# Kernel optimization log

Hardware: AMD Instinct MI355X
Metric: run time of the kernel (lower is better)

The kernel has to match this reference:

```python
import jax, jax.numpy as jnp
import numpy as np
from jax import lax

# program token ids
PAD, START, END, SCENE, INTERSECT, FILT, RELATE, QUERY = range(8)
SKIP = (PAD, START, END)


def conv2d(x, w, b, dil=1):
    # 'same' padding for odd kernels (3x3 pad=dil, 1x1 pad=0), NCHW/OIHW
    pad = dil * (w.shape[2] // 2)
    y = lax.conv_general_dilated(x, w, (1, 1), [(pad, pad), (pad, pad)],
                                 rhs_dilation=(dil, dil),
                                 dimension_numbers=('NCHW', 'OIHW', 'NCHW'))
    return y + b[None, :, None, None]


def maxpool2(x):
    return lax.reduce_window(x, -jnp.inf, lax.max, (1, 1, 2, 2), (1, 1, 2, 2), 'VALID')


def exec_program(prog, feat_input, p):
    """Run one (concrete) program over a batch of stem features. prog: tuple of ints,
    executed in reversed order exactly like TbDNet.forward."""
    B, _, H, W = feat_input.shape
    output = feat_input
    saved = None
    for t in reversed(prog):
        if t in SKIP:
            continue
        if t == SCENE:
            saved = output
            output = jnp.ones((B, 1, H, W), feat_input.dtype)
        elif t == INTERSECT:  # AndModule: elementwise min of attentions
            output = jnp.minimum(output, saved)
        elif t == FILT:
            a = feat_input * output  # [B,D,H,W] * [B,1,H,W]
            a = jax.nn.relu(conv2d(a, p['att_w1'], p['att_b1']))
            a = jax.nn.relu(conv2d(a, p['att_w2'], p['att_b2']))
            output = jax.nn.sigmoid(conv2d(a, p['att_w3'], p['att_b3']))
        elif t == RELATE:  # RelateModule: dilated conv stack (1,2,4,8,1) -> conv1x1 sigmoid
            a = feat_input * output
            for w, b, d in ((p['rel_w1'], p['rel_b1'], 1), (p['rel_w2'], p['rel_b2'], 2),
                            (p['rel_w3'], p['rel_b3'], 4), (p['rel_w4'], p['rel_b4'], 8),
                            (p['rel_w5'], p['rel_b5'], 1)):
                a = jax.nn.relu(conv2d(a, w, b, d))
            output = jax.nn.sigmoid(conv2d(a, p['rel_w6'], p['rel_b6']))
        elif t == QUERY:
            a = feat_input * output
            a = jax.nn.relu(conv2d(a, p['qry_w1'], p['qry_b1']))
            output = jax.nn.relu(conv2d(a, p['qry_w2'], p['qry_b2']))
    return output


def tbd_forward(feats, programs_np, p):
    B = feats.shape[0]
    stem = jax.nn.relu(conv2d(feats, p['stem_w1'], p['stem_b1']))
    stem = jax.nn.relu(conv2d(stem, p['stem_w2'], p['stem_b2']))  # [B,D,H,W]
    D, H, W = stem.shape[1], stem.shape[2], stem.shape[3]
    # group samples by identical program so dispatch runs batched, not per-sample
    groups = {}
    for n in range(B):
        groups.setdefault(tuple(int(v) for v in programs_np[n]), []).append(n)
    mod_out = jnp.zeros((B, D, H, W), feats.dtype)
    for prog, idxs in groups.items():
        idx = jnp.array(idxs)
        mod_out = mod_out.at[idx].set(exec_program(prog, stem[idx], p))
    # classifier: conv1x1 -> relu -> maxpool2 -> flatten -> fc -> relu -> fc
    x = jax.nn.relu(conv2d(mod_out, p['cls_w'], p['cls_b']))
    x = maxpool2(x)                        # [B,1024,7,7]
    x = x.reshape(B, -1)                   # [B,50176]
    x = jax.nn.relu(x @ p['fc1_w'].T + p['fc1_b'])
    return x @ p['fc2_w'].T + p['fc2_b']   # [B,28]


def setup_inputs() -> dict:
    key = jax.random.key(0)
    ks = iter(jax.random.split(key, 64))
    def rn(shape, s=0.05):
        return jax.random.normal(next(ks), shape, dtype=jnp.float32) * s
    B, Cin, H, W, D, P, L, A = 64, 1024, 14, 14, 128, 1024, 1024, 28
    feats = jax.random.normal(next(ks), (B, Cin, H, W), dtype=jnp.float32)
    # stored programs; execution order is reversed(stored)
    progA = [START, QUERY, FILT, RELATE, FILT, SCENE, END, PAD]            # scene->filter->relate->filter->query
    progB = [START, QUERY, INTERSECT, FILT, SCENE, FILT, SCENE, END]       # two filter branches -> intersect -> query
    programs = jnp.array([progA] * (B // 2) + [progB] * (B // 2), dtype=jnp.int32)
    inp = {'feats': feats, 'programs': programs,
           'stem_w1': rn((D, Cin, 3, 3), 0.02), 'stem_b1': rn((D,)),
           'stem_w2': rn((D, D, 3, 3)), 'stem_b2': rn((D,)),
           'att_w1': rn((D, D, 3, 3)), 'att_b1': rn((D,)),
           'att_w2': rn((D, D, 3, 3)), 'att_b2': rn((D,)),
           'att_w3': rn((1, D, 1, 1)), 'att_b3': rn((1,)),
           'rel_w1': rn((D, D, 3, 3)), 'rel_b1': rn((D,)),
           'rel_w2': rn((D, D, 3, 3)), 'rel_b2': rn((D,)),
           'rel_w3': rn((D, D, 3, 3)), 'rel_b3': rn((D,)),
           'rel_w4': rn((D, D, 3, 3)), 'rel_b4': rn((D,)),
           'rel_w5': rn((D, D, 3, 3)), 'rel_b5': rn((D,)),
           'rel_w6': rn((1, D, 1, 1)), 'rel_b6': rn((1,)),
           'qry_w1': rn((D, D, 3, 3)), 'qry_b1': rn((D,)),
           'qry_w2': rn((D, D, 3, 3)), 'qry_b2': rn((D,)),
           'cls_w': rn((P, D, 1, 1)), 'cls_b': rn((P,)),
           'fc1_w': rn((L, P * (H // 2) * (W // 2)), 0.01), 'fc1_b': rn((L,)),
           'fc2_w': rn((A, L)), 'fc2_b': rn((A,))}
    return inp


PARAM_NAMES = ['stem_w1', 'stem_b1', 'stem_w2', 'stem_b2',
               'att_w1', 'att_b1', 'att_w2', 'att_b2', 'att_w3', 'att_b3',
               'rel_w1', 'rel_b1', 'rel_w2', 'rel_b2', 'rel_w3', 'rel_b3',
               'rel_w4', 'rel_b4', 'rel_w5', 'rel_b5', 'rel_w6', 'rel_b6',
               'qry_w1', 'qry_b1', 'qry_w2', 'qry_b2',
               'cls_w', 'cls_b', 'fc1_w', 'fc1_b', 'fc2_w', 'fc2_b']


def reference(feats, programs, stem_w1, stem_b1, stem_w2, stem_b2,
              att_w1, att_b1, att_w2, att_b2, att_w3, att_b3,
              rel_w1, rel_b1, rel_w2, rel_b2, rel_w3, rel_b3,
              rel_w4, rel_b4, rel_w5, rel_b5, rel_w6, rel_b6,
              qry_w1, qry_b1, qry_w2, qry_b2,
              cls_w, cls_b, fc1_w, fc1_b, fc2_w, fc2_b):
    vals = [stem_w1, stem_b1, stem_w2, stem_b2,
            att_w1, att_b1, att_w2, att_b2, att_w3, att_b3,
            rel_w1, rel_b1, rel_w2, rel_b2, rel_w3, rel_b3,
            rel_w4, rel_b4, rel_w5, rel_b5, rel_w6, rel_b6,
            qry_w1, qry_b1, qry_w2, qry_b2,
            cls_w, cls_b, fc1_w, fc1_b, fc2_w, fc2_b]
    p = dict(zip(PARAM_NAMES, vals))
    return tbd_forward(feats, np.asarray(programs), p)
```

## Files before the change

kernel.cpp:

```cpp
#include <hip/hip_runtime.h>
#include <math.h>


typedef __attribute__((ext_vector_type(8)))  short   short8;
typedef __attribute__((ext_vector_type(8)))  __bf16  bf16x8;
typedef __attribute__((ext_vector_type(4)))  float   f32x4;

#define NROUNDS 8
#define NKS 98
#define S1KS 16

#define B_WSTEM1 0UL
#define B_WSTEM2 2359296UL
#define B_WMOD   2654208UL
#define B_WCLS   5308416UL
#define B_STEM   5570560UL
#define B_XA     8781824UL
#define B_XB     11993088UL
#define B_FEAT   15204352UL
#define B_ATTN   18415616UL
#define B_SAVED  18465792UL
#define B_SCHED  18515968UL
#define B_ACTB   18520064UL
#define B_FC1T   24942592UL
#define B_P1X1   25204736UL
#define B_S1P    67108864UL
#define B_FC1P   134217728UL

__device__ __forceinline__ unsigned short f2bf(float f) {
    __bf16 h = (__bf16)f;
    union { __bf16 h; unsigned short u; } c; c.h = h; return c.u;
}
__device__ __forceinline__ float bf2f(unsigned short u) {
    return __uint_as_float(((unsigned int)u) << 16);
}
__device__ __forceinline__ unsigned int pkbf(float a, float b) {
    return (unsigned int)f2bf(a) | ((unsigned int)f2bf(b) << 16);
}
__device__ __forceinline__ f32x4 mfma16(bf16x8 a, bf16x8 b, f32x4 c) {
    return __builtin_amdgcn_mfma_f32_16x16x32_bf16(a, b, c, 0, 0, 0);
}

struct PrepArgs { const float* src[12]; const int* prog; char* ws; };

__global__ __launch_bounds__(256) void k_prep(PrepArgs a)
{
    char* ws = a.ws;
    const int bx = blockIdx.x;
    if (bx < 768) {
        const int y = bx >> 6;
        const float* __restrict__ src = a.src[y];
        int gid = (bx & 63) * 256 + threadIdx.x;
        int gsz = 64 * 256;
        if (y == 11) {
            unsigned short* dst = (unsigned short*)(ws + B_WCLS);
            for (int i = gid; i < 131072; i += gsz) dst[i] = f2bf(src[i]);
        } else {
            const int IC = (y == 0) ? 1024 : 128;
            const int lg = (y == 0) ? 10 : 7;
            unsigned short* dst = (unsigned short*)(ws + ((y == 0) ? B_WSTEM1
                                        : (y == 1) ? B_WSTEM2
                                        : B_WMOD + (size_t)(y - 2) * 294912));
            const int total = 9 << (lg + 7);
            for (int i = gid; i < total; i += gsz) {
                int ic = i & (IC - 1);
                int oc = (i >> lg) & 127;
                int t  = i >> (lg + 7);
                dst[i] = f2bf(src[((size_t)oc * IC + ic) * 9 + t]);
            }
        }
        return;
    }
    int gid = (bx - 768) * 256 + threadIdx.x;
    int gsz = 256 * 256;
    float* attn  = (float*)(ws + B_ATTN);
    float* saved = (float*)(ws + B_SAVED);
    float* p1    = (float*)(ws + B_P1X1);
    for (int i = gid; i < 64 * 196; i += gsz) { attn[i] = 1.0f; saved[i] = 1.0f; }
    for (int i = gid; i < 8 * 64 * 196; i += gsz) p1[i] = 0.0f;
    unsigned int* fz = (unsigned int*)(ws + B_FEAT);
    for (int i = gid; i < 64 * 25088 / 2; i += gsz) fz[i] = 0u;
    if (gid < 64) {
        int n = gid;
        const int* prog = a.prog;
        int ent[NROUNDS];
        for (int r = 0; r < NROUNDS; ++r) ent[r] = 0;
        int rc = 0, nslot = 0;
        int pscene = 0, pinter = 0, pmat = 0, pmw = 0;
#define PREBITS ((pscene<<17)|(pinter<<18)|(pmat<<19)|(pmw<<22))
#define CLRPRE  (pscene = pinter = pmat = pmw = 0)
#define EMIT(v) do { if (rc < NROUNDS) ent[rc++] = (v); } while (0)
        for (int j = 7; j >= 0; --j) {
            int t = prog[n * 8 + j];
            switch (t) {
                case 3: pscene = 1; break;
                case 4: pinter = 1; break;
                case 5: {
                    int e1 = 5 | (0<<4) | (1<<8) | (1<<12) | (0<<15) | PREBITS
                               | (1<<23) | (0<<24) | (nslot<<25);
                    CLRPRE; EMIT(e1);
                    pmat = nslot + 1; pmw = 0; nslot++;
                    break;
                }
                case 6: {
                    int e1 = 3 | (2<<4) | (1<<8) | (1<<12) | (2<<13) | (0<<15) | PREBITS;
                    CLRPRE; EMIT(e1);
                    EMIT(3 | (3<<4) | (2<<8) | (0<<13) | (1<<15));
                    EMIT(3 | (4<<4) | (4<<8) | (1<<13) | (0<<15));
                    EMIT(3 | (5<<4) | (8<<8) | (0<<13) | (1<<15));
                    EMIT(3 | (6<<4) | (1<<8) | (1<<13) | (0<<15)
                           | (1<<23) | (1<<24) | (nslot<<25));
                    pmat = nslot + 1; pmw = 1; nslot++;
                    break;
                }
                case 7: {
                    int e1 = 5 | (7<<4) | (8<<8) | (1<<12) | (2<<15) | PREBITS;
                    CLRPRE; EMIT(e1);
                    break;
                }
                default: break;
            }
        }
#undef EMIT
#undef PREBITS
#undef CLRPRE
        int* sched = (int*)(ws + B_SCHED);
        for (int r = 0; r < NROUNDS; ++r) sched[n * NROUNDS + r] = ent[r];
    }
}

__global__ __launch_bounds__(512) void k_stem1p(const float* __restrict__ feats,
                                                const unsigned short* __restrict__ wrep,
                                                char* ws)
{
    __shared__ unsigned short s_img[197 * 72];
    const int bx = blockIdx.x;
    const int n = bx >> 4, ks = bx & 15;
    const int tid = threadIdx.x, lane = tid & 63;
    const int w = tid >> 6, wm = w & 1, wn = w >> 1;
    const int l15 = lane & 15, lq = lane >> 4;

    if (tid < 36) ((unsigned int*)(s_img + 196 * 72))[tid] = 0u;

    int pglob[4], pbyt[4], pyv[4], pxv[4];
#pragma unroll
    for (int j = 0; j < 4; ++j) {
        int p  = (wn + 4 * j) * 16 + l15;
        pglob[j] = p;
        int py = p / 14;
        pyv[j] = (p < 196) ? py : 10000;
        pxv[j] = p - py * 14;
        pbyt[j] = p * 144 + lq * 16;
    }
    const int zaddr = 196 * 144 + lq * 16;
    const int nJ = (wn == 0) ? 4 : 3;

    f32x4 acc[4][4];
#pragma unroll
    for (int m = 0; m < 4; ++m)
#pragma unroll
        for (int j = 0; j < 4; ++j) acc[m][j] = (f32x4){0.f, 0.f, 0.f, 0.f};

    const int icg = tid & 15;
    const int qq0 = tid >> 4;
    const int icb = ks * 64;

    const float* sf = feats + ((size_t)n * 1024 + icb) * 196;
    for (int qq = qq0; qq < 49; qq += 32) {
        const float* p0 = sf + icg * 4 * 196 + qq * 4;
        float4 r0 = *(const float4*)(p0);
        float4 r1 = *(const float4*)(p0 + 196);
        float4 r2 = *(const float4*)(p0 + 392);
        float4 r3 = *(const float4*)(p0 + 588);
#pragma unroll
        for (int e = 0; e < 4; ++e) {
            uint2 v;
            v.x = pkbf(((const float*)&r0)[e], ((const float*)&r1)[e]);
            v.y = pkbf(((const float*)&r2)[e], ((const float*)&r3)[e]);
            *(uint2*)(s_img + (qq * 4 + e) * 72 + icg * 4) = v;
        }
    }
    __syncthreads();

#pragma unroll
    for (int t = 0; t < 9; ++t) {
        const int dy = t / 3 - 1, dx = t % 3 - 1;
        int baddr[4];
#pragma unroll
        for (int j = 0; j < 4; ++j) {
            int yy = pyv[j] + dy, xx = pxv[j] + dx;
            bool ok = ((unsigned)yy < 14u) && ((unsigned)xx < 14u);
            baddr[j] = ok ? (pbyt[j] + (dy * 14 + dx) * 144) : zaddr;
        }
#pragma unroll
        for (int kc = 0; kc < 2; ++kc) {
            const unsigned short* wt = wrep +
                ((size_t)(t * 128 + wm * 64 + l15) * 1024 + icb + kc * 32 + lq * 8);
            bf16x8 am[4];
#pragma unroll
            for (int m = 0; m < 4; ++m)
                am[m] = *(const bf16x8*)(wt + (size_t)m * 16 * 1024);
#pragma unroll
            for (int j = 0; j < 4; ++j) {
                if (j < nJ) {
                    bf16x8 b = *(const bf16x8*)((const char*)s_img + baddr[j] + kc * 64);
#pragma unroll
                    for (int m = 0; m < 4; ++m)
                        acc[m][j] = mfma16(am[m], b, acc[m][j]);
                }
            }
        }
    }

    unsigned short* part = (unsigned short*)(ws + B_S1P);
#pragma unroll
    for (int m = 0; m < 4; ++m) {
        const int oc = wm * 64 + m * 16 + lq * 4;
#pragma unroll
        for (int j = 0; j < 4; ++j) {
            if (j < nJ) {
                int p = pglob[j];
                if (p < 196) {
                    uint2 pk;
                    pk.x = pkbf(acc[m][j][0], acc[m][j][1]);
                    pk.y = pkbf(acc[m][j][2], acc[m][j][3]);
                    *(uint2*)(part + (((size_t)ks * 64 + n) * 196 + p) * 128 + oc) = pk;
                }
            }
        }
    }
}

__global__ __launch_bounds__(256) void k_stem1r(const char* __restrict__ ws_c,
                                                const float* __restrict__ bias,
                                                unsigned short* __restrict__ xa)
{
    int i = blockIdx.x * 256 + threadIdx.x;
    const unsigned short* part = (const unsigned short*)(ws_c + B_S1P);
    int oc8 = (i & 15) * 8;
    int np  = i >> 4;
    float s[8] = {};
#pragma unroll
    for (int ks = 0; ks < S1KS; ++ks) {
        short8 v = *(const short8*)(part + (((size_t)ks * 64) * 196 + np) * 128 + oc8);
#pragma unroll
        for (int e = 0; e < 8; ++e) s[e] += bf2f((unsigned short)v[e]);
    }
    short8 o;
#pragma unroll
    for (int e = 0; e < 8; ++e)
        o[e] = (short)f2bf(fmaxf(s[e] + bias[oc8 + e], 0.f));
    *(short8*)(xa + (size_t)np * 128 + oc8) = o;
}

__device__ void conv_core32(const unsigned short* __restrict__ srcB,
                            const unsigned short* __restrict__ wrep,
                            const float* __restrict__ bias,
                            unsigned short* __restrict__ dst,
                            int oct, int pxh,
                            unsigned short* s_img)
{
    const int tid  = threadIdx.x, lane = tid & 63;
    const int w    = tid >> 6, wm = w & 1, wn = w >> 1;
    const int l15  = lane & 15, lq = lane >> 4;

    if (tid < 68) ((unsigned int*)s_img)[196 * 68 + tid] = 0u;

    int pglob[4], pbyt[4], pyv[4], pxv[4];
#pragma unroll
    for (int j = 0; j < 4; ++j) {
        int nt = wn + 2 * j;
        int p  = (pxh * 7 + nt) * 16 + l15;
        pglob[j] = p;
        int py = p / 14;
        pyv[j] = (p < 196) ? py : 10000;
        pxv[j] = p - py * 14;
        pbyt[j] = p * 272 + lq * 16;
    }
    const int zaddr = 196 * 272 + lq * 16;
    const int nNT = (wn == 0) ? 4 : 3;

    f32x4 acc[4];
#pragma unroll
    for (int j = 0; j < 4; ++j) acc[j] = (f32x4){0.f, 0.f, 0.f, 0.f};

    for (int i = tid; i < 196 * 16; i += 256) {
        int p = i >> 4, c8 = (i & 15) * 8;
        *(short8*)(s_img + p * 136 + c8) = *(const short8*)(srcB + p * 128 + c8);
    }
    __syncthreads();

    const unsigned short* wlane = wrep + (size_t)(oct * 32 + wm * 16 + l15) * 128 + lq * 8;
#pragma unroll
    for (int t = 0; t < 9; ++t) {
        const int dy = t / 3 - 1, dx = t % 3 - 1;
        int baddr[4];
#pragma unroll
        for (int j = 0; j < 4; ++j) {
            int yy = pyv[j] + dy, xx = pxv[j] + dx;
            bool ok = ((unsigned)yy < 14u) && ((unsigned)xx < 14u);
            baddr[j] = ok ? (pbyt[j] + (dy * 14 + dx) * 272) : zaddr;
        }
        const unsigned short* wt = wlane + (size_t)(t * 128) * 128;
#pragma unroll
        for (int kc = 0; kc < 4; ++kc) {
            bf16x8 a0 = *(const bf16x8*)(wt + kc * 32);
#pragma unroll
            for (int j = 0; j < 4; ++j) {
                if (j < nNT) {
                    bf16x8 b = *(const bf16x8*)((const char*)s_img + baddr[j] + kc * 64);
                    acc[j] = mfma16(a0, b, acc[j]);
                }
            }
        }
    }

    const int oc = oct * 32 + wm * 16 + lq * 4;
    const float4 b4 = *(const float4*)(bias + oc);
#pragma unroll
    for (int j = 0; j < 4; ++j) {
        if (j < nNT) {
            int p = pglob[j];
            if (p < 196) {
                uint2 pk;
                pk.x = pkbf(fmaxf(acc[j][0] + b4.x, 0.f), fmaxf(acc[j][1] + b4.y, 0.f));
                pk.y = pkbf(fmaxf(acc[j][2] + b4.z, 0.f), fmaxf(acc[j][3] + b4.w, 0.f));
                *(uint2*)(dst + p * 128 + oc) = pk;
            }
        }
    }
}

__global__ __launch_bounds__(256) void k_conv_stem2(const unsigned short* __restrict__ srcBall,
                                                    const unsigned short* __restrict__ wrep,
                                                    const float* __restrict__ bias,
                                                    unsigned short* __restrict__ dstall)
{
    __shared__ unsigned short s_img[197 * 136];
    const int n = blockIdx.x >> 3, oct = (blockIdx.x >> 1) & 3, pxh = blockIdx.x & 1;
    conv_core32(srcBall + (size_t)n * 25088, wrep, bias,
                dstall + (size_t)n * 25088, oct, pxh, s_img);
}

struct RArgs {
    char* ws;
    const float* mbias[9];
    const float* w1x1[2];
    const float* b1x1[2];
};

__global__ __launch_bounds__(512) void k_round(RArgs a, int r)
{
    __shared__ unsigned short s_img[197 * 136];
    __shared__ unsigned short s_tmp[197 * 136];
    __shared__ float s_gate[196];
    const int bx = blockIdx.x;
    const int n = bx >> 2, oct = bx & 3;
    char* ws = a.ws;
    const int* sched = (const int*)(ws + B_SCHED);
    const int e = sched[n * NROUNDS + r];
    const int op = e & 15;
    if (op == 0) return;
    const int tid = threadIdx.x, lane = tid & 63;
    const int w = tid >> 6, wm = w & 1, wn = w >> 1;
    const int l15 = lane & 15, lq = lane >> 4;
    const int wset1 = (e >> 4) & 15, f8 = (e >> 8) & 15, gatef = (e >> 12) & 1;
    const int srcid = (e >> 13) & 3, dstid = (e >> 15) & 3;
    const int fscene = (e >> 17) & 1, finter = (e >> 18) & 1;
    const int mslot = (e >> 19) & 7, mw = (e >> 22) & 1;
    const int post = (e >> 23) & 1, pw = (e >> 24) & 1, pslot = (e >> 25) & 7;

    float* attn  = (float*)(ws + B_ATTN)  + n * 196;
    float* saved = (float*)(ws + B_SAVED) + n * 196;
    float* p1    = (float*)(ws + B_P1X1);

    if (tid < 68) ((unsigned int*)s_img)[196 * 68 + tid] = 0u;
    else if (tid < 136) ((unsigned int*)s_tmp)[196 * 68 + (tid - 68)] = 0u;

    if (gatef && tid < 196) {
        float cur = attn[tid];
        if (mslot) {
            float pv = p1[(size_t)(mslot - 1) * 12544 + n * 196 + tid];
            cur = 1.0f / (1.0f + __expf(-(pv + a.b1x1[mw][0])));
        }
        if (fscene) { saved[tid] = cur; cur = 1.0f; }
        if (finter) { cur = fminf(cur, saved[tid]); }
        if (mslot | fscene | finter) attn[tid] = cur;
        s_gate[tid] = cur;
    }
    __syncthreads();

    const int zaddr = 196 * 272 + lq * 16;
    const unsigned short* wmod = (const unsigned short*)(ws + B_WMOD);

    if (op == 3) {
        const unsigned short* src = (const unsigned short*)(ws +
                (srcid == 2 ? B_STEM : srcid == 1 ? B_XB : B_XA)) + (size_t)n * 25088;
        if (gatef) {
            for (int i = tid; i < 196 * 16; i += 512) {
                int p = i >> 4, c8 = (i & 15) * 8;
                short8 v = *(const short8*)(src + p * 128 + c8);
                float g = s_gate[p];
                uint2 o0, o1;
                o0.x = pkbf(bf2f((unsigned short)v[0]) * g, bf2f((unsigned short)v[1]) * g);
                o0.y = pkbf(bf2f((unsigned short)v[2]) * g, bf2f((unsigned short)v[3]) * g);
                o1.x = pkbf(bf2f((unsigned short)v[4]) * g, bf2f((unsigned short)v[5]) * g);
                o1.y = pkbf(bf2f((unsigned short)v[6]) * g, bf2f((unsigned short)v[7]) * g);
                *(uint2*)(s_img + p * 136 + c8)     = o0;
                *(uint2*)(s_img + p * 136 + c8 + 4) = o1;
            }
        } else {
            for (int i = tid; i < 196 * 16; i += 512) {
                int p = i >> 4, c8 = (i & 15) * 8;
                *(short8*)(s_img + p * 136 + c8) = *(const short8*)(src + p * 128 + c8);
            }
        }
        __syncthreads();

        int pglob[4], pbyt[4], pyv[4], pxv[4];
#pragma unroll
        for (int j = 0; j < 4; ++j) {
            int p = (wn + 4 * j) * 16 + l15;
            pglob[j] = p;
            int py = p / 14;
            pyv[j] = (p < 196) ? py : 10000;
            pxv[j] = p - py * 14;
            pbyt[j] = p * 272 + lq * 16;
        }
        const int nJ = (wn == 0) ? 4 : 3;
        f32x4 acc[4];
#pragma unroll
        for (int j = 0; j < 4; ++j) acc[j] = (f32x4){0.f, 0.f, 0.f, 0.f};

        const int dil = f8;
        const unsigned short* wlane = wmod + (size_t)wset1 * 147456 / 2 * 0;
        wlane = wmod + (size_t)wset1 * 9 * 128 * 128
                     + (size_t)(oct * 32 + wm * 16 + l15) * 128 + lq * 8;
#pragma unroll
        for (int t = 0; t < 9; ++t) {
            const int dy = (t / 3 - 1) * dil, dx = (t % 3 - 1) * dil;
            int ba[4];
#pragma unroll
            for (int j = 0; j < 4; ++j) {
                int yy = pyv[j] + dy, xx = pxv[j] + dx;
                bool ok = ((unsigned)yy < 14u) && ((unsigned)xx < 14u);
                ba[j] = ok ? (pbyt[j] + (dy * 14 + dx) * 272) : zaddr;
            }
            const unsigned short* wt = wlane + (size_t)(t * 128) * 128;
#pragma unroll
            for (int kc = 0; kc < 4; ++kc) {
                bf16x8 a0 = *(const bf16x8*)(wt + kc * 32);
#pragma unroll
                for (int j = 0; j < 4; ++j) {
                    if (j < nJ) {
                        bf16x8 b = *(const bf16x8*)((const char*)s_img + ba[j] + kc * 64);
                        acc[j] = mfma16(a0, b, acc[j]);
                    }
                }
            }
        }

        unsigned short* dst = (unsigned short*)(ws +
                (dstid == 2 ? B_FEAT : dstid == 1 ? B_XB : B_XA)) + (size_t)n * 25088;
        const int oc = oct * 32 + wm * 16 + lq * 4;
        const float4 b4 = *(const float4*)(a.mbias[wset1] + oc);
        float4 wv4;
        if (post) wv4 = *(const float4*)(a.w1x1[pw] + oc);
        float* pdst = p1 + (size_t)pslot * 12544 + n * 196;
#pragma unroll
        for (int j = 0; j < 4; ++j) {
            if (j < nJ) {
                int p = pglob[j];
                if (p < 196) {
                    float v0 = fmaxf(acc[j][0] + b4.x, 0.f);
                    float v1 = fmaxf(acc[j][1] + b4.y, 0.f);
                    float v2 = fmaxf(acc[j][2] + b4.z, 0.f);
                    float v3 = fmaxf(acc[j][3] + b4.w, 0.f);
                    uint2 pk; pk.x = pkbf(v0, v1); pk.y = pkbf(v2, v3);
                    *(uint2*)(dst + p * 128 + oc) = pk;
                    if (post)
                        atomicAdd(pdst + p, v0 * wv4.x + v1 * wv4.y + v2 * wv4.z + v3 * wv4.w);
                }
            }
        }
    } else {
        const unsigned short* stem = (const unsigned short*)(ws + B_STEM) + (size_t)n * 25088;
        for (int i = tid; i < 196 * 16; i += 512) {
            int p = i >> 4, c8 = (i & 15) * 8;
            short8 v = *(const short8*)(stem + p * 128 + c8);
            float g = s_gate[p];
            uint2 o0, o1;
            o0.x = pkbf(bf2f((unsigned short)v[0]) * g, bf2f((unsigned short)v[1]) * g);
            o0.y = pkbf(bf2f((unsigned short)v[2]) * g, bf2f((unsigned short)v[3]) * g);
            o1.x = pkbf(bf2f((unsigned short)v[4]) * g, bf2f((unsigned short)v[5]) * g);
            o1.y = pkbf(bf2f((unsigned short)v[6]) * g, bf2f((unsigned short)v[7]) * g);
            *(uint2*)(s_img + p * 136 + c8)     = o0;
            *(uint2*)(s_img + p * 136 + c8 + 4) = o1;
        }
        __syncthreads();

        const unsigned short* w1 = wmod + (size_t)wset1 * 9 * 128 * 128;
        int pg2[13], pb2[13], pyv2[13], pxv2[13];
#pragma unroll
        for (int j2 = 0; j2 < 13; ++j2) {
            int p = j2 * 16 + l15;
            pg2[j2] = p;
            int py = p / 14;
            pyv2[j2] = (p < 196) ? py : 10000;
            pxv2[j2] = p - py * 14;
            pb2[j2] = p * 272 + lq * 16;
        }
        f32x4 acc1[13];
#pragma unroll
        for (int j2 = 0; j2 < 13; ++j2) acc1[j2] = (f32x4){0.f, 0.f, 0.f, 0.f};
#pragma unroll
        for (int t = 0; t < 9; ++t) {
            const int dy = t / 3 - 1, dx = t % 3 - 1;
            int ba[13];
#pragma unroll
            for (int j2 = 0; j2 < 13; ++j2) {
                int yy = pyv2[j2] + dy, xx = pxv2[j2] + dx;
                bool ok = ((unsigned)yy < 14u) && ((unsigned)xx < 14u);
                ba[j2] = ok ? (pb2[j2] + (dy * 14 + dx) * 272) : zaddr;
            }
#pragma unroll
            for (int kc = 0; kc < 4; ++kc) {
                bf16x8 av = *(const bf16x8*)(w1 +
                    (size_t)(t * 128 + w * 16 + l15) * 128 + kc * 32 + lq * 8);
#pragma unroll
                for (int j2 = 0; j2 < 13; ++j2) {
                    bf16x8 b = *(const bf16x8*)((const char*)s_img + ba[j2] + kc * 64);
                    acc1[j2] = mfma16(av, b, acc1[j2]);
                }
            }
        }
        {
            const int oc1 = w * 16 + lq * 4;
            const float4 b14 = *(const float4*)(a.mbias[wset1] + oc1);
#pragma unroll
            for (int j2 = 0; j2 < 13; ++j2) {
                int p = pg2[j2];
                if (p < 196) {
                    uint2 pk;
                    pk.x = pkbf(fmaxf(acc1[j2][0] + b14.x, 0.f),
                                fmaxf(acc1[j2][1] + b14.y, 0.f));
                    pk.y = pkbf(fmaxf(acc1[j2][2] + b14.z, 0.f),
                                fmaxf(acc1[j2][3] + b14.w, 0.f));
                    *(uint2*)(s_tmp + p * 136 + oc1) = pk;
                }
            }
        }
        __syncthreads();

        const unsigned short* w2base = wmod + (size_t)f8 * 9 * 128 * 128
                     + (size_t)(oct * 32 + wm * 16 + l15) * 128 + lq * 8;
        int pglob[4], pbyt[4], pyv[4], pxv[4];
#pragma unroll
        for (int j = 0; j < 4; ++j) {
            int p = (wn + 4 * j) * 16 + l15;
            pglob[j] = p;
            int py = p / 14;
            pyv[j] = (p < 196) ? py : 10000;
            pxv[j] = p - py * 14;
            pbyt[j] = p * 272 + lq * 16;
        }
        const int nJ = (wn == 0) ? 4 : 3;
        f32x4 acc[4];
#pragma unroll
        for (int j = 0; j < 4; ++j) acc[j] = (f32x4){0.f, 0.f, 0.f, 0.f};
#pragma unroll
        for (int t = 0; t < 9; ++t) {
            const int dy = t / 3 - 1, dx = t % 3 - 1;
            int ba[4];
#pragma unroll
            for (int j = 0; j < 4; ++j) {
                int yy = pyv[j] + dy, xx = pxv[j] + dx;
                bool ok = ((unsigned)yy < 14u) && ((unsigned)xx < 14u);
                ba[j] = ok ? (pbyt[j] + (dy * 14 + dx) * 272) : zaddr;
            }
            const unsigned short* wt = w2base + (size_t)(t * 128) * 128;
#pragma unroll
            for (int kc = 0; kc < 4; ++kc) {
                bf16x8 a0 = *(const bf16x8*)(wt + kc * 32);
#pragma unroll
                for (int j = 0; j < 4; ++j) {
                    if (j < nJ) {
                        bf16x8 b = *(const bf16x8*)((const char*)s_tmp + ba[j] + kc * 64);
                        acc[j] = mfma16(a0, b, acc[j]);
                    }
                }
            }
        }
        const int oc = oct * 32 + wm * 16 + lq * 4;
        const float4 b24 = *(const float4*)(a.mbias[f8] + oc);
        unsigned short* feat = (unsigned short*)(ws + B_FEAT) + (size_t)n * 25088;
        float4 wv4;
        if (post) wv4 = *(const float4*)(a.w1x1[pw] + oc);
        float* pdst = p1 + (size_t)pslot * 12544 + n * 196;
#pragma unroll
        for (int j = 0; j < 4; ++j) {
            if (j < nJ) {
                int p = pglob[j];
                if (p < 196) {
                    float v0 = fmaxf(acc[j][0] + b24.x, 0.f);
                    float v1 = fmaxf(acc[j][1] + b24.y, 0.f);
                    float v2 = fmaxf(acc[j][2] + b24.z, 0.f);
                    float v3 = fmaxf(acc[j][3] + b24.w, 0.f);
                    if (dstid == 2) {
                        uint2 pk; pk.x = pkbf(v0, v1); pk.y = pkbf(v2, v3);
                        *(uint2*)(feat + p * 128 + oc) = pk;
                    }
                    if (post)
                        atomicAdd(pdst + p, v0 * wv4.x + v1 * wv4.y + v2 * wv4.z + v3 * wv4.w);
                }
            }
        }
    }
}

__global__ __launch_bounds__(256) void k_cls_pool(const unsigned short* __restrict__ featall,
                                                  const unsigned short* __restrict__ clsw,
                                                  const float* __restrict__ clsb,
                                                  unsigned short* __restrict__ actB)
{
    __shared__ char smem[197 * 272 + 64 * 200 * 4];
    unsigned short* s_img = (unsigned short*)smem;
    float* s_pool = (float*)(smem + 197 * 272);
    const int n = blockIdx.x >> 4, pt = blockIdx.x & 15;
    const int tid = threadIdx.x, lane = tid & 63, w = tid >> 6;
    const int l15 = lane & 15, lq = lane >> 4;
    const unsigned short* feat = featall + (size_t)n * 25088;

    if (tid < 68) ((unsigned int*)s_img)[196 * 68 + tid] = 0u;
    for (int i = tid; i < 196 * 16; i += 256) {
        int p = i >> 4, c8 = (i & 15) * 8;
        *(short8*)(s_img + p * 136 + c8) = *(const short8*)(feat + p * 128 + c8);
    }
    f32x4 acc[14];
#pragma unroll
    for (int j = 0; j < 14; ++j) acc[j] = (f32x4){0.f, 0.f, 0.f, 0.f};
    __syncthreads();

    const unsigned short* wl = clsw + (size_t)(pt * 64 + w * 16 + l15) * 128 + lq * 8;
#pragma unroll
    for (int kc = 0; kc < 4; ++kc) {
        bf16x8 a0 = *(const bf16x8*)(wl + kc * 32);
#pragma unroll
        for (int j = 0; j < 14; ++j) {
            int p = j * 16 + l15;
            int ba = (p < 196) ? (p * 272 + lq * 16 + kc * 64) : (196 * 272 + lq * 16);
            bf16x8 b = *(const bf16x8*)((const char*)s_img + ba);
            acc[j] = mfma16(a0, b, acc[j]);
        }
    }
    const int oc = pt * 64 + w * 16 + lq * 4;
    const float4 b4 = *(const float4*)(clsb + oc);
    const int pl = w * 16 + lq * 4;
#pragma unroll
    for (int j = 0; j < 14; ++j) {
        int p = j * 16 + l15;
        if (p < 196) {
            s_pool[(pl + 0) * 200 + p] = fmaxf(acc[j][0] + b4.x, 0.f);
            s_pool[(pl + 1) * 200 + p] = fmaxf(acc[j][1] + b4.y, 0.f);
            s_pool[(pl + 2) * 200 + p] = fmaxf(acc[j][2] + b4.z, 0.f);
            s_pool[(pl + 3) * 200 + p] = fmaxf(acc[j][3] + b4.w, 0.f);
        }
    }
    __syncthreads();
    for (int i = tid; i < 64 * 49; i += 256) {
        int plx = i / 49, q = i - plx * 49;
        int py = q / 7, qx = q - py * 7;
        const float* rp = s_pool + plx * 200 + py * 28 + qx * 2;
        float m = fmaxf(fmaxf(rp[0], rp[1]), fmaxf(rp[14], rp[15]));
        int k = (pt * 64 + plx) * 49 + q;
        int kb = k >> 6, lq2 = (k >> 4) & 3, hi = (k >> 3) & 1, e = k & 7;
        actB[((((size_t)kb * 4 + lq2) * 2 + hi) * 64 + n) * 8 + e] = f2bf(m);
    }
}

__global__ __launch_bounds__(256) void k_fc1p(const unsigned short* __restrict__ actB,
                                              const float* __restrict__ w,
                                              float* __restrict__ part)
{
    __shared__ unsigned short s_w[64 * 264];
    const int jt = blockIdx.x & 15, ks = blockIdx.x >> 4;
    const int tid = threadIdx.x, lane = tid & 63, wv = tid >> 6;
    const int l15 = lane & 15, lq = lane >> 4;
    const int k0 = ks * 512;

    f32x4 acc[4];
#pragma unroll
    for (int t = 0; t < 4; ++t) acc[t] = (f32x4){0.f, 0.f, 0.f, 0.f};

    float4 pf[16];

#define FC1_LOAD(ss_) do {                                                        \
    _Pragma("unroll")                                                             \
    for (int pass = 0; pass < 16; ++pass) {                                       \
        const int row_ = pass * 4 + wv;                                           \
        pf[pass] = *(const float4*)(w + (size_t)(jt * 64 + row_) * 50176 + k0     \
                                      + (ss_) * 256 + lane * 4);                  \
    } } while (0)

    FC1_LOAD(0);

    for (int ss = 0; ss < 2; ++ss) {
        __syncthreads();
#pragma unroll
        for (int pass = 0; pass < 16; ++pass) {
            const int row = pass * 4 + wv;
            uint2 v;
            v.x = pkbf(pf[pass].x, pf[pass].y);
            v.y = pkbf(pf[pass].z, pf[pass].w);
            *(uint2*)(s_w + row * 264 + lane * 4) = v;
        }
        __syncthreads();
        if (ss < 1) FC1_LOAD(1);

        const unsigned short* arow = s_w + (wv * 16 + l15) * 264;
#pragma unroll
        for (int kk = 0; kk < 8; ++kk) {
            bf16x8 a = *(const bf16x8*)(arow + kk * 32 + lq * 8);
            const int kglob = k0 + ss * 256 + kk * 32 + lq * 8;
            const int kb = kglob >> 6, lq2 = (kglob >> 4) & 3, hi = (kglob >> 3) & 1;
            const unsigned short* bp = actB +
                ((((size_t)kb * 4 + lq2) * 2 + hi) * 64 + l15) * 8;
#pragma unroll
            for (int t = 0; t < 4; ++t) {
                bf16x8 b = *(const bf16x8*)(bp + t * 128);
                acc[t] = mfma16(a, b, acc[t]);
            }
        }
    }
#undef FC1_LOAD

    float* pbase = part + ((size_t)ks * 1024 + jt * 64 + wv * 16 + lq * 4) * 64 + l15;
#pragma unroll
    for (int t = 0; t < 4; ++t)
#pragma unroll
        for (int r = 0; r < 4; ++r)
            pbase[(size_t)r * 64 + t * 16] = acc[t][r];
}

__global__ __launch_bounds__(256) void k_fc1r(const float* __restrict__ part,
                                              const float* __restrict__ b,
                                              float* __restrict__ fc1T)
{
    int i = blockIdx.x * 256 + threadIdx.x;
    if (i >= 65536) return;
    float s = 0.0f;
    for (int ks = 0; ks < NKS; ++ks) s += part[(size_t)ks * 65536 + i];
    int j = i >> 6;
    fc1T[i] = fmaxf(s + b[j], 0.0f);
}

__global__ __launch_bounds__(256) void k_fc2(const float* __restrict__ fc1T,
                                             const float* __restrict__ w,
                                             const float* __restrict__ b,
                                             float* __restrict__ out)
{
    __shared__ float red[256];
    const int a_ = blockIdx.x;
    const int tid = threadIdx.x, lane = tid & 63, q = tid >> 6;
    float acc = 0.0f;
    const float* wr = w + (size_t)a_ * 1024;
    for (int k = q * 256; k < q * 256 + 256; ++k)
        acc = fmaf(fc1T[k * 64 + lane], wr[k], acc);
    red[tid] = acc;
    __syncthreads();
    if (q == 0) {
        float s = red[tid] + red[tid + 64] + red[tid + 128] + red[tid + 192] + b[a_];
        out[lane * 28 + a_] = s;
    }
}

extern "C" void kernel_launch(void* const* d_in, const int* in_sizes, int n_in,
                              void* d_out, int out_size, void* d_ws, size_t ws_size,
                              hipStream_t stream)
{
    const float* feats = (const float*)d_in[0];
    const int*   prog  = (const int*)d_in[1];
    char* ws  = (char*)d_ws;
    float* out = (float*)d_out;

    PrepArgs pa;
    pa.src[0]  = (const float*)d_in[2];
    pa.src[1]  = (const float*)d_in[4];
    pa.src[2]  = (const float*)d_in[6];
    pa.src[3]  = (const float*)d_in[8];
    pa.src[4]  = (const float*)d_in[12];
    pa.src[5]  = (const float*)d_in[14];
    pa.src[6]  = (const float*)d_in[16];
    pa.src[7]  = (const float*)d_in[18];
    pa.src[8]  = (const float*)d_in[20];
    pa.src[9]  = (const float*)d_in[24];
    pa.src[10] = (const float*)d_in[26];
    pa.src[11] = (const float*)d_in[28];
    pa.prog = prog;
    pa.ws = ws;
    k_prep<<<1024, 256, 0, stream>>>(pa);

    k_stem1p<<<1024, 512, 0, stream>>>(feats, (const unsigned short*)(ws + B_WSTEM1), ws);
    k_stem1r<<<784, 256, 0, stream>>>(ws, (const float*)d_in[3],
                                      (unsigned short*)(ws + B_XA));

    k_conv_stem2<<<512, 256, 0, stream>>>((const unsigned short*)(ws + B_XA),
                                          (const unsigned short*)(ws + B_WSTEM2),
                                          (const float*)d_in[5],
                                          (unsigned short*)(ws + B_STEM));

    RArgs ga;
    ga.ws = ws;
    ga.mbias[0] = (const float*)d_in[7];
    ga.mbias[1] = (const float*)d_in[9];
    ga.mbias[2] = (const float*)d_in[13];
    ga.mbias[3] = (const float*)d_in[15];
    ga.mbias[4] = (const float*)d_in[17];
    ga.mbias[5] = (const float*)d_in[19];
    ga.mbias[6] = (const float*)d_in[21];
    ga.mbias[7] = (const float*)d_in[25];
    ga.mbias[8] = (const float*)d_in[27];
    ga.w1x1[0]  = (const float*)d_in[10];
    ga.w1x1[1]  = (const float*)d_in[22];
    ga.b1x1[0]  = (const float*)d_in[11];
    ga.b1x1[1]  = (const float*)d_in[23];

    for (int r = 0; r < NROUNDS; ++r)
        k_round<<<256, 512, 0, stream>>>(ga, r);

    k_cls_pool<<<1024, 256, 0, stream>>>((const unsigned short*)(ws + B_FEAT),
                                         (const unsigned short*)(ws + B_WCLS),
                                         (const float*)d_in[29],
                                         (unsigned short*)(ws + B_ACTB));
    k_fc1p<<<1568, 256, 0, stream>>>((const unsigned short*)(ws + B_ACTB),
                                     (const float*)d_in[30], (float*)(ws + B_FC1P));
    k_fc1r<<<256, 256, 0, stream>>>((const float*)(ws + B_FC1P), (const float*)d_in[31],
                                    (float*)(ws + B_FC1T));
    k_fc2<<<28, 256, 0, stream>>>((const float*)(ws + B_FC1T), (const float*)d_in[32],
                                  (const float*)d_in[33], out);
}
```

Measured before the change: 511.8 us.

## Pre-transpose stem features to bf16 pixel-major and halve stem1 K-splits

Adds a transpose kernel that converts the NCHW fp32 input features into a pixel-major bf16 layout in the workspace. The first stem conv then loads its 128-channel slab with plain vector copies instead of converting and transposing per block. It also doubles the channels per block, halving the K-split count from 16 to 8 and shrinking the partial-sum reduction traffic. The cost is an extra kernel launch and an extra pass writing and reading the feature tensor, plus fewer, heavier blocks with more LDS each.

```diff
diff --git a/kernel.cpp b/kernel.cpp
--- a/kernel.cpp
+++ b/kernel.cpp
@@ -8,7 +8,7 @@
 
 #define NROUNDS 8
 #define NKS 98
-#define S1KS 16
+#define S1KS 8
 
 #define B_WSTEM1 0UL
 #define B_WSTEM2 2359296UL
@@ -24,6 +24,7 @@
 #define B_ACTB   18520064UL
 #define B_FC1T   24942592UL
 #define B_P1X1   25204736UL
+#define B_FT     33554432UL
 #define B_S1P    67108864UL
 #define B_FC1P   134217728UL
 
@@ -39,6 +40,33 @@
 }
 __device__ __forceinline__ f32x4 mfma16(bf16x8 a, bf16x8 b, f32x4 c) {
     return __builtin_amdgcn_mfma_f32_16x16x32_bf16(a, b, c, 0, 0, 0);
+}
+
+__global__ __launch_bounds__(256) void k_tr(const float* __restrict__ feats,
+                                            unsigned short* __restrict__ ft)
+{
+    __shared__ float s[32 * 201];
+    const int n = blockIdx.x >> 5, it = blockIdx.x & 31;
+    const int tid = threadIdx.x, lane = tid & 63, w = tid >> 6;
+    const float* src = feats + ((size_t)n * 1024 + it * 32) * 196;
+
+    for (int r = w; r < 32; r += 4) {
+        if (lane < 49) {
+            float4 v = *(const float4*)(src + r * 196 + lane * 4);
+            float* sr = s + r * 201 + lane * 4;
+            sr[0] = v.x; sr[1] = v.y; sr[2] = v.z; sr[3] = v.w;
+        }
+    }
+    __syncthreads();
+
+    const int ic4 = (tid & 7) * 4;
+    unsigned short* dst = ft + (size_t)n * 200704 + it * 32 + ic4;
+    for (int p = tid >> 3; p < 196; p += 32) {
+        uint2 v;
+        v.x = pkbf(s[(ic4 + 0) * 201 + p], s[(ic4 + 1) * 201 + p]);
+        v.y = pkbf(s[(ic4 + 2) * 201 + p], s[(ic4 + 3) * 201 + p]);
+        *(uint2*)(dst + (size_t)p * 1024) = v;
+    }
 }
 
 struct PrepArgs { const float* src[12]; const int* prog; char* ws; };
@@ -129,18 +157,25 @@
     }
 }
 
-__global__ __launch_bounds__(512) void k_stem1p(const float* __restrict__ feats,
+__global__ __launch_bounds__(512) void k_stem1p(const unsigned short* __restrict__ ft,
                                                 const unsigned short* __restrict__ wrep,
                                                 char* ws)
 {
-    __shared__ unsigned short s_img[197 * 72];
+    __shared__ unsigned short s_img[197 * 136];
     const int bx = blockIdx.x;
-    const int n = bx >> 4, ks = bx & 15;
+    const int n = bx >> 3, ks = bx & 7;
     const int tid = threadIdx.x, lane = tid & 63;
     const int w = tid >> 6, wm = w & 1, wn = w >> 1;
     const int l15 = lane & 15, lq = lane >> 4;
-
-    if (tid < 36) ((unsigned int*)(s_img + 196 * 72))[tid] = 0u;
+    const int icb = ks * 128;
+
+    if (tid < 68) ((unsigned int*)s_img)[196 * 68 + tid] = 0u;
+
+    const unsigned short* slab = ft + (size_t)n * 200704 + icb;
+    for (int i = tid; i < 196 * 16; i += 512) {
+        int p = i >> 4, c8 = (i & 15) * 8;
+        *(short8*)(s_img + p * 136 + c8) = *(const short8*)(slab + (size_t)p * 1024 + c8);
+    }
 
     int pglob[4], pbyt[4], pyv[4], pxv[4];
 #pragma unroll
@@ -150,9 +185,9 @@
         int py = p / 14;
         pyv[j] = (p < 196) ? py : 10000;
         pxv[j] = p - py * 14;
-        pbyt[j] = p * 144 + lq * 16;
-    }
-    const int zaddr = 196 * 144 + lq * 16;
+        pbyt[j] = p * 272 + lq * 16;
+    }
+    const int zaddr = 196 * 272 + lq * 16;
     const int nJ = (wn == 0) ? 4 : 3;
 
     f32x4 acc[4][4];
@@ -160,26 +195,6 @@
     for (int m = 0; m < 4; ++m)
 #pragma unroll
         for (int j = 0; j < 4; ++j) acc[m][j] = (f32x4){0.f, 0.f, 0.f, 0.f};
-
-    const int icg = tid & 15;
-    const int qq0 = tid >> 4;
-    const int icb = ks * 64;
-
-    const float* sf = feats + ((size_t)n * 1024 + icb) * 196;
-    for (int qq = qq0; qq < 49; qq += 32) {
-        const float* p0 = sf + icg * 4 * 196 + qq * 4;
-        float4 r0 = *(const float4*)(p0);
-        float4 r1 = *(const float4*)(p0 + 196);
-        float4 r2 = *(const float4*)(p0 + 392);
-        float4 r3 = *(const float4*)(p0 + 588);
-#pragma unroll
-        for (int e = 0; e < 4; ++e) {
-            uint2 v;
-            v.x = pkbf(((const float*)&r0)[e], ((const float*)&r1)[e]);
-            v.y = pkbf(((const float*)&r2)[e], ((const float*)&r3)[e]);
-            *(uint2*)(s_img + (qq * 4 + e) * 72 + icg * 4) = v;
-        }
-    }
     __syncthreads();
 
 #pragma unroll
@@ -190,10 +205,10 @@
         for (int j = 0; j < 4; ++j) {
             int yy = pyv[j] + dy, xx = pxv[j] + dx;
             bool ok = ((unsigned)yy < 14u) && ((unsigned)xx < 14u);
-            baddr[j] = ok ? (pbyt[j] + (dy * 14 + dx) * 144) : zaddr;
-        }
-#pragma unroll
-        for (int kc = 0; kc < 2; ++kc) {
+            baddr[j] = ok ? (pbyt[j] + (dy * 14 + dx) * 272) : zaddr;
+        }
+#pragma unroll
+        for (int kc = 0; kc < 4; ++kc) {
             const unsigned short* wt = wrep +
                 ((size_t)(t * 128 + wm * 64 + l15) * 1024 + icb + kc * 32 + lq * 8);
             bf16x8 am[4];
@@ -433,8 +448,7 @@
         for (int j = 0; j < 4; ++j) acc[j] = (f32x4){0.f, 0.f, 0.f, 0.f};
 
         const int dil = f8;
-        const unsigned short* wlane = wmod + (size_t)wset1 * 147456 / 2 * 0;
-        wlane = wmod + (size_t)wset1 * 9 * 128 * 128
+        const unsigned short* wlane = wmod + (size_t)wset1 * 9 * 128 * 128
                      + (size_t)(oct * 32 + wm * 16 + l15) * 128 + lq * 8;
 #pragma unroll
         for (int t = 0; t < 9; ++t) {
@@ -782,6 +796,8 @@
     const int*   prog  = (const int*)d_in[1];
     char* ws  = (char*)d_ws;
     float* out = (float*)d_out;
+
+    k_tr<<<2048, 256, 0, stream>>>(feats, (unsigned short*)(ws + B_FT));
 
     PrepArgs pa;
     pa.src[0]  = (const float*)d_in[2];
@@ -800,7 +816,8 @@
     pa.ws = ws;
     k_prep<<<1024, 256, 0, stream>>>(pa);
 
-    k_stem1p<<<1024, 512, 0, stream>>>(feats, (const unsigned short*)(ws + B_WSTEM1), ws);
+    k_stem1p<<<512, 512, 0, stream>>>((const unsigned short*)(ws + B_FT),
+                                      (const unsigned short*)(ws + B_WSTEM1), ws);
     k_stem1r<<<784, 256, 0, stream>>>(ws, (const float*)d_in[3],
                                       (unsigned short*)(ws + B_XA));
 
```

After: 514.3 us. Within noise of the previous version (+0.5%).
